# Kernel tuning notes

Hardware: AMD Instinct MI355X
Metric: run time of the kernel (lower is better)

## Reference

```python
import jax, jax.numpy as jnp
import numpy as np

B, T, C, H = 8, 2048, 1024, 64  # batch, seq (block_size), n_embd, head_size


def setup_inputs() -> dict:
    key = jax.random.key(0)
    kx, kq, kk, kv = jax.random.split(key, 4)
    s = 1.0 / np.sqrt(C)
    return {
        "x": jax.random.normal(kx, (B, T, C), dtype=jnp.float32),
        "Wq": jax.random.normal(kq, (C, H), dtype=jnp.float32) * s,
        "Wk": jax.random.normal(kk, (C, H), dtype=jnp.float32) * s,
        "Wv": jax.random.normal(kv, (C, H), dtype=jnp.float32) * s,
    }


def reference(x, Wq, Wk, Wv):
    t = x.shape[1]
    q = jnp.einsum("btc,ch->bth", x, Wq)
    k = jnp.einsum("btc,ch->bth", x, Wk)
    v = jnp.einsum("btc,ch->bth", x, Wv)
    scores = jnp.einsum("bqh,bkh->bqk", q, k) / jnp.sqrt(jnp.float32(H))
    causal = jnp.tril(jnp.ones((t, t), dtype=bool))  # tril mask
    scores = jnp.where(causal, scores, -jnp.inf)
    attn = jax.nn.softmax(scores, axis=-1)
    return jnp.einsum("bqk,bkh->bqh", attn, v)
```

## Files before the change

### kernel.cpp

```cpp
#include <hip/hip_runtime.h>
#include <hip/hip_bf16.h>

#define BB 8
#define TT 2048
#define CC 1024
#define HH 64

typedef __attribute__((ext_vector_type(8)))  short bf16x8;
typedef __attribute__((ext_vector_type(4)))  float f32x4;
typedef __attribute__((ext_vector_type(16))) float f32x16;
typedef __attribute__((ext_vector_type(8)))  unsigned short us8;
typedef unsigned int u32;

static __device__ __forceinline__ unsigned short f2bf(float f) {
    union { float f; unsigned int u; } v; v.f = f;
    unsigned int u = v.u;
    return (unsigned short)((u + 0x7FFFu + ((u >> 16) & 1u)) >> 16);
}

__global__ __launch_bounds__(256) void prep_weights(
        const float* __restrict__ Wq, const float* __restrict__ Wk,
        const float* __restrict__ Wv, unsigned short* __restrict__ Wt) {
    __shared__ float tile[64][65];
    int w  = blockIdx.x >> 4;
    int c0 = (blockIdx.x & 15) * 64;
    const float* W = (w == 0) ? Wq : (w == 1) ? Wk : Wv;
    int li = threadIdx.x;
    {
        int c = li >> 2, h4 = (li & 3) * 16;
        const float* src = W + (size_t)(c0 + c) * HH + h4;
        #pragma unroll
        for (int i = 0; i < 4; ++i) {
            float4 v4 = *(const float4*)(src + i * 4);
            tile[c][h4 + i*4 + 0] = v4.x; tile[c][h4 + i*4 + 1] = v4.y;
            tile[c][h4 + i*4 + 2] = v4.z; tile[c][h4 + i*4 + 3] = v4.w;
        }
    }
    __syncthreads();
    float scale = (w == 0) ? 0.1803368802f : 1.0f;
    int h = li >> 2, cg = (li & 3) * 16;
    unsigned short* dst = Wt + (size_t)w * HH * CC + (size_t)h * CC + c0 + cg;
    #pragma unroll
    for (int i = 0; i < 16; ++i) dst[i] = f2bf(tile[cg + i][h] * scale);
}

__global__ __launch_bounds__(512, 4) void proj_qkv(
        const float* __restrict__ x, const unsigned short* __restrict__ Wt,
        unsigned short* __restrict__ qws, unsigned short* __restrict__ kws,
        unsigned short* __restrict__ vws) {
    __shared__ unsigned short Xs[2][32 * 64];
    __shared__ unsigned short Ws[2][192 * 64];
    int tid = threadIdx.x;
    int wv = tid >> 6, lane = tid & 63;
    int quad = (lane >> 4) & 3, lq = lane & 15;
    int mg = wv >> 2, ng = wv & 3;
    int r0 = blockIdx.x * 32;

    bool xact = tid < 256;
    int xr = tid >> 3, xg = tid & 7;
    const float* xsrc = x + (size_t)(r0 + xr) * CC + xg * 8;
    int xdst = xr * 64 + ((xg ^ (xr & 7)) * 8);
    float4 xa, xb;

    f32x4 acc[3];
    #pragma unroll
    for (int nt = 0; nt < 3; ++nt)
        #pragma unroll
        for (int i = 0; i < 4; ++i) acc[nt][i] = 0.0f;

    auto stageW = [&](int buf, int kc) {
        #pragma unroll
        for (int i = 0; i < 3; ++i) {
            int fp = tid + i * 512;
            int r = fp >> 3, pb = fp & 7, g = pb ^ (r & 7);
            const u32 __attribute__((address_space(1)))* gsrc =
                (const u32 __attribute__((address_space(1)))*)
                    (Wt + (size_t)r * CC + kc * 64 + g * 8);
            u32 __attribute__((address_space(3)))* ldst =
                (u32 __attribute__((address_space(3)))*)(&Ws[buf][fp * 8]);
            __builtin_amdgcn_global_load_lds(gsrc, ldst, 16, 0, 0);
        }
    };
    auto loadX = [&](int kc) {
        xa = *(const float4*)(xsrc + kc * 64);
        xb = *(const float4*)(xsrc + kc * 64 + 4);
    };
    auto writeX = [&](int buf) {
        unsigned short h[8];
        h[0]=f2bf(xa.x); h[1]=f2bf(xa.y); h[2]=f2bf(xa.z); h[3]=f2bf(xa.w);
        h[4]=f2bf(xb.x); h[5]=f2bf(xb.y); h[6]=f2bf(xb.z); h[7]=f2bf(xb.w);
        *(us8*)&Xs[buf][xdst] = *(const us8*)h;
    };

    if (xact) loadX(0);
    stageW(0, 0);
    if (xact) writeX(0);

    for (int kc = 0; kc < 16; ++kc) {
        int cur = kc & 1;
        __syncthreads();
        if (kc < 15) {
            if (xact) loadX(kc + 1);
            stageW(1 - cur, kc + 1);
        }
        #pragma unroll
        for (int ks = 0; ks < 2; ++ks) {
            int g = ks * 4 + quad;
            int arow = mg * 16 + lq;
            bf16x8 a = *(const bf16x8*)&Xs[cur][arow * 64 + (g ^ (lq & 7)) * 8];
            bf16x8 b[3];
            #pragma unroll
            for (int nt = 0; nt < 3; ++nt) {
                int brow = ng * 48 + nt * 16 + lq;
                b[nt] = *(const bf16x8*)&Ws[cur][brow * 64 + (g ^ (lq & 7)) * 8];
            }
            #pragma unroll
            for (int nt = 0; nt < 3; ++nt)
                acc[nt] = __builtin_amdgcn_mfma_f32_16x16x32_bf16(
                    a, b[nt], acc[nt], 0, 0, 0);
        }
        if (kc < 15 && xact) writeX(1 - cur);
    }

    #pragma unroll
    for (int nt = 0; nt < 3; ++nt) {
        int g = ng * 48 + nt * 16 + lq;
        #pragma unroll
        for (int i = 0; i < 4; ++i) {
            int row = r0 + mg * 16 + quad * 4 + i;
            unsigned short bv = f2bf(acc[nt][i]);
            if (g < 64)       qws[(size_t)row * HH + g] = bv;
            else if (g < 128) kws[(size_t)row * HH + (g - 64)] = bv;
            else              vws[((size_t)(row >> 11) * HH + (g - 128)) * TT
                                  + (row & (TT - 1))] = bv;
        }
    }
}

__global__ __launch_bounds__(64, 4) void attn(
        const unsigned short* __restrict__ qws,
        const unsigned short* __restrict__ kws,
        const unsigned short* __restrict__ vws,
        float* __restrict__ out, float* __restrict__ Lat) {
    __shared__ unsigned short Kt[32][72];
    __shared__ unsigned short Vt[64][40];
    __shared__ unsigned short Ps[32][40];
    int ti = blockIdx.x;
    int s  = blockIdx.y;
    int b  = blockIdx.z;
    if (ti < s) return;
    int lane = threadIdx.x, half = lane >> 5, l31 = lane & 31;

    bf16x8 qf[4];
    {
        const unsigned short* qp =
            qws + ((size_t)b * TT + ti * 32 + l31) * HH + half * 8;
        #pragma unroll
        for (int ks = 0; ks < 4; ++ks) qf[ks] = *(const bf16x8*)(qp + ks * 16);
    }
    f32x16 O0, O1, Lc;
    #pragma unroll
    for (int i = 0; i < 16; ++i) { O0[i] = 0.f; O1[i] = 0.f; Lc[i] = 0.f; }
    bf16x8 ones;
    #pragma unroll
    for (int i = 0; i < 8; ++i) ones[i] = (short)0x3F80;

    for (int jc = s; jc <= ti; jc += 4) {
        __syncthreads();
        #pragma unroll
        for (int i = 0; i < 4; ++i) {
            int slot = i * 64 + lane;
            int r = slot >> 3, g = slot & 7;
            *(us8*)&Kt[r][g * 8] =
                *(const us8*)(kws + ((size_t)b * TT + jc * 32 + r) * HH + g * 8);
        }
        #pragma unroll
        for (int i = 0; i < 4; ++i) {
            int slot = i * 64 + lane;
            int h = slot >> 2, kb = slot & 3;
            *(us8*)&Vt[h][kb * 8] =
                *(const us8*)(vws + ((size_t)b * HH + h) * TT + jc * 32 + kb * 8);
        }
        __syncthreads();
        f32x16 S;
        #pragma unroll
        for (int i = 0; i < 16; ++i) S[i] = 0.f;
        #pragma unroll
        for (int ks = 0; ks < 4; ++ks) {
            bf16x8 kf = *(const bf16x8*)&Kt[l31][ks * 16 + half * 8];
            S = __builtin_amdgcn_mfma_f32_32x32x16_bf16(qf[ks], kf, S, 0, 0, 0);
        }
        bool diag = (jc == ti);
        #pragma unroll
        for (int r = 0; r < 16; ++r) {
            int row = (r & 3) + 8 * (r >> 2) + 4 * half;
            float p = __builtin_amdgcn_exp2f(S[r]);
            if (diag && l31 > row) p = 0.0f;
            Ps[row][l31] = f2bf(p);
        }
        __syncthreads();
        #pragma unroll
        for (int ks = 0; ks < 2; ++ks) {
            bf16x8 pa  = *(const bf16x8*)&Ps[l31][ks * 16 + half * 8];
            bf16x8 vf0 = *(const bf16x8*)&Vt[l31][ks * 16 + half * 8];
            bf16x8 vf1 = *(const bf16x8*)&Vt[32 + l31][ks * 16 + half * 8];
            O0 = __builtin_amdgcn_mfma_f32_32x32x16_bf16(pa, vf0, O0, 0, 0, 0);
            O1 = __builtin_amdgcn_mfma_f32_32x32x16_bf16(pa, vf1, O1, 0, 0, 0);
            Lc = __builtin_amdgcn_mfma_f32_32x32x16_bf16(pa, ones, Lc, 0, 0, 0);
        }
    }
    float* Ob = out + ((size_t)b * TT + ti * 32) * HH;
    #pragma unroll
    for (int r = 0; r < 16; ++r) {
        int row = (r & 3) + 8 * (r >> 2) + 4 * half;
        atomicAdd(Ob + (size_t)row * HH + l31,      O0[r]);
        atomicAdd(Ob + (size_t)row * HH + 32 + l31, O1[r]);
    }
    if (l31 == 0) {
        #pragma unroll
        for (int r = 0; r < 16; ++r) {
            int row = (r & 3) + 8 * (r >> 2) + 4 * half;
            atomicAdd(Lat + (size_t)b * TT + ti * 32 + row, Lc[r]);
        }
    }
}

__global__ __launch_bounds__(256) void norm_out(
        float* __restrict__ out, const float* __restrict__ Lat) {
    int idx = blockIdx.x * 256 + threadIdx.x;
    float inv = 1.0f / Lat[idx >> 4];
    float4* o4 = (float4*)out;
    float4 v = o4[idx];
    v.x *= inv; v.y *= inv; v.z *= inv; v.w *= inv;
    o4[idx] = v;
}

extern "C" void kernel_launch(void* const* d_in, const int* in_sizes, int n_in,
                              void* d_out, int out_size, void* d_ws, size_t ws_size,
                              hipStream_t stream) {
    (void)in_sizes; (void)n_in; (void)out_size; (void)ws_size;
    const float* x  = (const float*)d_in[0];
    const float* Wq = (const float*)d_in[1];
    const float* Wk = (const float*)d_in[2];
    const float* Wv = (const float*)d_in[3];
    float* out = (float*)d_out;

    char* ws = (char*)d_ws;
    unsigned short* Wt  = (unsigned short*)ws;
    unsigned short* qws = (unsigned short*)(ws + (1u << 19));
    unsigned short* kws = (unsigned short*)(ws + (1u << 19) + (1u << 21));
    unsigned short* vws = (unsigned short*)(ws + (1u << 19) + (2u << 21));
    float*          Lat = (float*)       (ws + (1u << 19) + (3u << 21));

    prep_weights<<<48, 256, 0, stream>>>(Wq, Wk, Wv, Wt);
    hipMemsetAsync(out, 0, (size_t)BB * TT * HH * sizeof(float), stream);
    hipMemsetAsync(Lat, 0, (size_t)BB * TT * sizeof(float), stream);
    proj_qkv<<<512, 512, 0, stream>>>(x, Wt, qws, kws, vws);
    attn<<<dim3(64, 4, 8), 64, 0, stream>>>(qws, kws, vws, out, Lat);
    norm_out<<<1024, 256, 0, stream>>>(out, Lat);
}
```

Before: 147.2 us.

## Widen attention blocks, replace atomics with split-K partials, stage V transpose

Attention blocks now hold two waves covering 64 query rows, so each K/V tile loaded into shared memory is reused by both waves. The atomicAdd accumulation into out and Lat is replaced by per-split partial buffers, which norm_out sums and normalizes; this also removes both memsets. The projection kernel prefetches X two chunks ahead and transposes V through shared memory so it can be written with coalesced vector stores instead of scattered scalar stores. The costs are extra workspace traffic for the partial buffers and fewer, larger attention blocks.

```diff
diff --git a/kernel.cpp b/kernel.cpp
--- a/kernel.cpp
+++ b/kernel.cpp
@@ -60,7 +60,7 @@
     int xr = tid >> 3, xg = tid & 7;
     const float* xsrc = x + (size_t)(r0 + xr) * CC + xg * 8;
     int xdst = xr * 64 + ((xg ^ (xr & 7)) * 8);
-    float4 xa, xb;
+    float4 xa[2], xb[2];
 
     f32x4 acc[3];
     #pragma unroll
@@ -81,28 +81,28 @@
             __builtin_amdgcn_global_load_lds(gsrc, ldst, 16, 0, 0);
         }
     };
-    auto loadX = [&](int kc) {
-        xa = *(const float4*)(xsrc + kc * 64);
-        xb = *(const float4*)(xsrc + kc * 64 + 4);
+    auto loadX = [&](int set, int kc) {
+        xa[set] = *(const float4*)(xsrc + kc * 64);
+        xb[set] = *(const float4*)(xsrc + kc * 64 + 4);
     };
-    auto writeX = [&](int buf) {
+    auto writeX = [&](int set, int buf) {
         unsigned short h[8];
-        h[0]=f2bf(xa.x); h[1]=f2bf(xa.y); h[2]=f2bf(xa.z); h[3]=f2bf(xa.w);
-        h[4]=f2bf(xb.x); h[5]=f2bf(xb.y); h[6]=f2bf(xb.z); h[7]=f2bf(xb.w);
+        h[0]=f2bf(xa[set].x); h[1]=f2bf(xa[set].y);
+        h[2]=f2bf(xa[set].z); h[3]=f2bf(xa[set].w);
+        h[4]=f2bf(xb[set].x); h[5]=f2bf(xb[set].y);
+        h[6]=f2bf(xb[set].z); h[7]=f2bf(xb[set].w);
         *(us8*)&Xs[buf][xdst] = *(const us8*)h;
     };
 
-    if (xact) loadX(0);
+    if (xact) { loadX(0, 0); loadX(1, 1); }
     stageW(0, 0);
-    if (xact) writeX(0);
+    if (xact) writeX(0, 0);
 
     for (int kc = 0; kc < 16; ++kc) {
         int cur = kc & 1;
         __syncthreads();
-        if (kc < 15) {
-            if (xact) loadX(kc + 1);
-            stageW(1 - cur, kc + 1);
-        }
+        if (kc < 15) stageW(1 - cur, kc + 1);
+        if (xact && kc < 14) loadX(kc & 1, kc + 2);
         #pragma unroll
         for (int ks = 0; ks < 2; ++ks) {
             int g = ks * 4 + quad;
@@ -119,42 +119,52 @@
                 acc[nt] = __builtin_amdgcn_mfma_f32_16x16x32_bf16(
                     a, b[nt], acc[nt], 0, 0, 0);
         }
-        if (kc < 15 && xact) writeX(1 - cur);
-    }
-
+        if (xact && kc < 15) writeX((kc + 1) & 1, 1 - cur);
+    }
+
+    __syncthreads();
+    unsigned short* Vl = (unsigned short*)Xs;
     #pragma unroll
     for (int nt = 0; nt < 3; ++nt) {
         int g = ng * 48 + nt * 16 + lq;
         #pragma unroll
         for (int i = 0; i < 4; ++i) {
-            int row = r0 + mg * 16 + quad * 4 + i;
+            int row = mg * 16 + quad * 4 + i;
             unsigned short bv = f2bf(acc[nt][i]);
-            if (g < 64)       qws[(size_t)row * HH + g] = bv;
-            else if (g < 128) kws[(size_t)row * HH + (g - 64)] = bv;
-            else              vws[((size_t)(row >> 11) * HH + (g - 128)) * TT
-                                  + (row & (TT - 1))] = bv;
-        }
-    }
-}
-
-__global__ __launch_bounds__(64, 4) void attn(
+            if (g < 64)       qws[(size_t)(r0 + row) * HH + g] = bv;
+            else if (g < 128) kws[(size_t)(r0 + row) * HH + (g - 64)] = bv;
+            else              Vl[(g - 128) * 36 + row] = bv;
+        }
+    }
+    __syncthreads();
+    if (tid < 256) {
+        int h = tid >> 2, tb = (tid & 3) * 8;
+        int b = r0 >> 11, rr = r0 & (TT - 1);
+        *(us8*)(vws + ((size_t)b * HH + h) * TT + rr + tb) =
+            *(const us8*)&Vl[h * 36 + tb];
+    }
+}
+
+__global__ __launch_bounds__(128, 3) void attn(
         const unsigned short* __restrict__ qws,
         const unsigned short* __restrict__ kws,
         const unsigned short* __restrict__ vws,
-        float* __restrict__ out, float* __restrict__ Lat) {
+        float* __restrict__ Op, float* __restrict__ Lp) {
     __shared__ unsigned short Kt[32][72];
     __shared__ unsigned short Vt[64][40];
-    __shared__ unsigned short Ps[32][40];
+    __shared__ unsigned short Ps[64][40];
     int ti = blockIdx.x;
     int s  = blockIdx.y;
     int b  = blockIdx.z;
-    if (ti < s) return;
-    int lane = threadIdx.x, half = lane >> 5, l31 = lane & 31;
+    int last = 2 * ti + 1;
+    if (s > last) return;
+    int tid = threadIdx.x, wv = tid >> 6, lane = tid & 63;
+    int half = lane >> 5, l31 = lane & 31;
 
     bf16x8 qf[4];
     {
         const unsigned short* qp =
-            qws + ((size_t)b * TT + ti * 32 + l31) * HH + half * 8;
+            qws + ((size_t)b * TT + ti * 64 + wv * 32 + l31) * HH + half * 8;
         #pragma unroll
         for (int ks = 0; ks < 4; ++ks) qf[ks] = *(const bf16x8*)(qp + ks * 16);
     }
@@ -165,18 +175,18 @@
     #pragma unroll
     for (int i = 0; i < 8; ++i) ones[i] = (short)0x3F80;
 
-    for (int jc = s; jc <= ti; jc += 4) {
+    for (int jc = s; jc <= last; jc += 4) {
         __syncthreads();
         #pragma unroll
-        for (int i = 0; i < 4; ++i) {
-            int slot = i * 64 + lane;
+        for (int i = 0; i < 2; ++i) {
+            int slot = tid + i * 128;
             int r = slot >> 3, g = slot & 7;
             *(us8*)&Kt[r][g * 8] =
                 *(const us8*)(kws + ((size_t)b * TT + jc * 32 + r) * HH + g * 8);
         }
         #pragma unroll
-        for (int i = 0; i < 4; ++i) {
-            int slot = i * 64 + lane;
+        for (int i = 0; i < 2; ++i) {
+            int slot = tid + i * 128;
             int h = slot >> 2, kb = slot & 3;
             *(us8*)&Vt[h][kb * 8] =
                 *(const us8*)(vws + ((size_t)b * HH + h) * TT + jc * 32 + kb * 8);
@@ -190,18 +200,17 @@
             bf16x8 kf = *(const bf16x8*)&Kt[l31][ks * 16 + half * 8];
             S = __builtin_amdgcn_mfma_f32_32x32x16_bf16(qf[ks], kf, S, 0, 0, 0);
         }
-        bool diag = (jc == ti);
+        bool diag = (jc >= 2 * ti + wv);
         #pragma unroll
         for (int r = 0; r < 16; ++r) {
-            int row = (r & 3) + 8 * (r >> 2) + 4 * half;
+            int pat = (r & 3) + 8 * (r >> 2) + 4 * half;
             float p = __builtin_amdgcn_exp2f(S[r]);
-            if (diag && l31 > row) p = 0.0f;
-            Ps[row][l31] = f2bf(p);
-        }
-        __syncthreads();
+            if (diag && jc * 32 + l31 > ti * 64 + wv * 32 + pat) p = 0.0f;
+            Ps[wv * 32 + pat][l31] = f2bf(p);
+        }
         #pragma unroll
         for (int ks = 0; ks < 2; ++ks) {
-            bf16x8 pa  = *(const bf16x8*)&Ps[l31][ks * 16 + half * 8];
+            bf16x8 pa  = *(const bf16x8*)&Ps[wv * 32 + l31][ks * 16 + half * 8];
             bf16x8 vf0 = *(const bf16x8*)&Vt[l31][ks * 16 + half * 8];
             bf16x8 vf1 = *(const bf16x8*)&Vt[32 + l31][ks * 16 + half * 8];
             O0 = __builtin_amdgcn_mfma_f32_32x32x16_bf16(pa, vf0, O0, 0, 0, 0);
@@ -209,30 +218,39 @@
             Lc = __builtin_amdgcn_mfma_f32_32x32x16_bf16(pa, ones, Lc, 0, 0, 0);
         }
     }
-    float* Ob = out + ((size_t)b * TT + ti * 32) * HH;
+    float* Ob = Op + (((size_t)s * BB + b) * TT + ti * 64 + wv * 32) * HH;
     #pragma unroll
     for (int r = 0; r < 16; ++r) {
-        int row = (r & 3) + 8 * (r >> 2) + 4 * half;
-        atomicAdd(Ob + (size_t)row * HH + l31,      O0[r]);
-        atomicAdd(Ob + (size_t)row * HH + 32 + l31, O1[r]);
+        int pat = (r & 3) + 8 * (r >> 2) + 4 * half;
+        Ob[(size_t)pat * HH + l31]      = O0[r];
+        Ob[(size_t)pat * HH + 32 + l31] = O1[r];
     }
     if (l31 == 0) {
         #pragma unroll
         for (int r = 0; r < 16; ++r) {
-            int row = (r & 3) + 8 * (r >> 2) + 4 * half;
-            atomicAdd(Lat + (size_t)b * TT + ti * 32 + row, Lc[r]);
+            int pat = (r & 3) + 8 * (r >> 2) + 4 * half;
+            Lp[((size_t)s * BB + b) * TT + ti * 64 + wv * 32 + pat] = Lc[r];
         }
     }
 }
 
 __global__ __launch_bounds__(256) void norm_out(
-        float* __restrict__ out, const float* __restrict__ Lat) {
+        const float* __restrict__ Op, const float* __restrict__ Lp,
+        float* __restrict__ out) {
     int idx = blockIdx.x * 256 + threadIdx.x;
-    float inv = 1.0f / Lat[idx >> 4];
-    float4* o4 = (float4*)out;
-    float4 v = o4[idx];
-    v.x *= inv; v.y *= inv; v.z *= inv; v.w *= inv;
-    o4[idx] = v;
+    int g = idx >> 4;
+    int ti = (g & (TT - 1)) >> 6;
+    int ns = min(2 * ti + 2, 4);
+    float4 a = make_float4(0.f, 0.f, 0.f, 0.f);
+    float Ls = 0.f;
+    for (int s = 0; s < ns; ++s) {
+        float4 v = ((const float4*)(Op + ((size_t)s * BB * TT + g) * HH))[idx & 15];
+        a.x += v.x; a.y += v.y; a.z += v.z; a.w += v.w;
+        Ls += Lp[(size_t)s * BB * TT + g];
+    }
+    float inv = 1.0f / Ls;
+    a.x *= inv; a.y *= inv; a.z *= inv; a.w *= inv;
+    ((float4*)out)[idx] = a;
 }
 
 extern "C" void kernel_launch(void* const* d_in, const int* in_sizes, int n_in,
@@ -250,12 +268,11 @@
     unsigned short* qws = (unsigned short*)(ws + (1u << 19));
     unsigned short* kws = (unsigned short*)(ws + (1u << 19) + (1u << 21));
     unsigned short* vws = (unsigned short*)(ws + (1u << 19) + (2u << 21));
-    float*          Lat = (float*)       (ws + (1u << 19) + (3u << 21));
+    float*          Op  = (float*)(ws + (1u << 19) + (3u << 21));
+    float*          Lp  = (float*)(ws + (1u << 19) + (3u << 21) + (1u << 24));
 
     prep_weights<<<48, 256, 0, stream>>>(Wq, Wk, Wv, Wt);
-    hipMemsetAsync(out, 0, (size_t)BB * TT * HH * sizeof(float), stream);
-    hipMemsetAsync(Lat, 0, (size_t)BB * TT * sizeof(float), stream);
     proj_qkv<<<512, 512, 0, stream>>>(x, Wt, qws, kws, vws);
-    attn<<<dim3(64, 4, 8), 64, 0, stream>>>(qws, kws, vws, out, Lat);
-    norm_out<<<1024, 256, 0, stream>>>(out, Lat);
-}
+    attn<<<dim3(32, 4, 8), 128, 0, stream>>>(qws, kws, vws, Op, Lp);
+    norm_out<<<1024, 256, 0, stream>>>(Op, Lp, out);
+}
```

Measured after the change: 138.2 us. 6.1% less time.
